# Performance work log

Hardware: AMD Instinct MI355X
Metric: run time of the kernel (lower is better)

## Reference

```python
import jax, jax.numpy as jnp
import numpy as np

# single species, e3tb basis 1s+1p+1d
FLIST = [1, 3, 5]           # flistnorbs (spin_factor = 1 pre-doubling)
NORB = 9                    # full_basis_norb
SPIN = 2                    # spin_deg -> block doubled
A, E, K = 192, 3072, 4
P = 58                      # sum_{i<=j} iorb*jorb = 1+3+5+9+15+25


def setup_inputs() -> dict:
    key = jax.random.key(0)
    ks = jax.random.split(key, 6)
    return dict(
        orbpair_hopping=jax.random.normal(ks[0], (E, P), jnp.float32),
        orbpair_onsite=jax.random.normal(ks[1], (A, P), jnp.float32),
        R_matrix=jax.random.normal(ks[2], (A, SPIN * NORB, SPIN * NORB), jnp.float32) * 0.1,
        kpoints=jax.random.uniform(ks[3], (K, 3), jnp.float32),
        edge_cell_shift=jax.random.normal(ks[4], (E, 3), jnp.float32),
        edge_index=jax.random.randint(ks[5], (2, E), 0, A, jnp.int64),
    )


def _assemble(feats):
    """Scatter flat orbpair features into upper-triangular [*, NORB, NORB] blocks."""
    n = feats.shape[0]
    H = jnp.zeros((n, NORB, NORB), feats.dtype)
    offs = np.concatenate([[0], np.cumsum(FLIST)])
    p = 0
    for i in range(len(FLIST)):
        for j in range(i, len(FLIST)):
            io, jo = FLIST[i], FLIST[j]
            f = 0.5 if i == j else 1.0  # diagonal orbpairs get 0.5 (hermitianized later)
            H = H.at[:, offs[i]:offs[i] + io, offs[j]:offs[j] + jo].set(
                f * feats[:, p:p + io * jo].reshape(n, io, jo))
            p += io * jo
    return H


def _spin_double(H):
    # H[:, :, 0, :, 0] = H[:, :, 1, :, 1] = H  (kron with eye(2), interleaved layout)
    n = H.shape[0]
    return jnp.einsum('aij,st->aisjt', H, jnp.eye(2, dtype=H.dtype)).reshape(n, SPIN * NORB, SPIN * NORB)


def reference(orbpair_hopping, orbpair_onsite, R_matrix, kpoints, edge_cell_shift, edge_index):
    s = SPIN * NORB
    src, dst = edge_index[0], edge_index[1]

    onsite = _spin_double(_assemble(orbpair_onsite))      # [A, s, s]
    hop = _spin_double(_assemble(orbpair_hopping))        # [E, s, s]

    # rotate: R @ H @ R^T (gathered per-edge for hoppings)
    onsite = jnp.einsum('aip,apq,ajq->aij', R_matrix, onsite, R_matrix)
    hop = jnp.einsum('eip,epq,ejq->eij', R_matrix[src], hop, R_matrix[dst])

    # Bloch phases exp(-2*pi*i k.S) per (k, edge)
    phase = jnp.exp(-2j * jnp.pi * (kpoints @ edge_cell_shift.T)).astype(jnp.complex64)  # [K, E]

    contrib = hop[None].astype(jnp.complex64) * phase[:, :, None, None]  # [K, E, s, s]
    pair = src * A + dst
    blk = jax.vmap(lambda c: jax.ops.segment_sum(c, pair, num_segments=A * A))(contrib)
    blk = blk.reshape(K, A, A, s, s)

    idx = jnp.arange(A)
    blk = blk.at[:, idx, idx].add(onsite[None].astype(jnp.complex64))  # onsite on diag, all k

    Hk = blk.transpose(0, 1, 3, 2, 4).reshape(K, A * s, A * s)
    return Hk + jnp.conj(jnp.swapaxes(Hk, 1, 2))
```

## Files before the change

kernel.cpp:

```cpp
#include <hip/hip_runtime.h>

#define PFEAT 58
#define S18   18
#define ENT   324
#define MAXE  128
#define MAXA  256

__device__ __constant__ unsigned char c_row[PFEAT] = {
    0,0,0,0,0,0,0,0,0,
    1,1,1,2,2,2,3,3,3,
    1,1,1,1,1,2,2,2,2,2,3,3,3,3,3,
    4,4,4,4,4,5,5,5,5,5,6,6,6,6,6,7,7,7,7,7,8,8,8,8,8};
__device__ __constant__ unsigned char c_col[PFEAT] = {
    0,1,2,3,4,5,6,7,8,
    1,2,3,1,2,3,1,2,3,
    4,5,6,7,8,4,5,6,7,8,4,5,6,7,8,
    4,5,6,7,8,4,5,6,7,8,4,5,6,7,8,4,5,6,7,8,4,5,6,7,8};
__device__ __constant__ float c_fac[PFEAT] = {
    0.5f,1,1,1,1,1,1,1,1,
    0.5f,0.5f,0.5f,0.5f,0.5f,0.5f,0.5f,0.5f,0.5f,
    1,1,1,1,1,1,1,1,1,1,1,1,1,1,1,
    0.5f,0.5f,0.5f,0.5f,0.5f,0.5f,0.5f,0.5f,0.5f,0.5f,0.5f,0.5f,0.5f,
    0.5f,0.5f,0.5f,0.5f,0.5f,0.5f,0.5f,0.5f,0.5f,0.5f,0.5f,0.5f};

__device__ __forceinline__ bool detect_i64(const int* __restrict__ ei) {
    const uint2* p = (const uint2*)ei;
    unsigned acc = 0u;
#pragma unroll 8
    for (int m = 0; m < 64; ++m) acc |= p[m].y;
    return acc == 0u;
}

__device__ __forceinline__ int load_idx(const int* __restrict__ ei, int pos,
                                        bool is64, int A) {
    int v = is64 ? ei[2 * pos] : ei[pos];
    v = v < 0 ? 0 : (v >= A ? A - 1 : v);
    return v;
}

__device__ __forceinline__ void assemble_rotate(
    const float* __restrict__ feat, const float* __restrict__ Rs,
    const float* __restrict__ Rd, float* sH9, float* sRs, float* sRd,
    float* sT, float* sM, int t, int nthreads)
{
    for (int idx = t; idx < ENT; idx += nthreads) { sRs[idx] = Rs[idx]; sRd[idx] = Rd[idx]; }
    if (t < 81) sH9[t] = 0.f;
    __syncthreads();
    if (t < PFEAT) sH9[c_row[t] * 9 + c_col[t]] = c_fac[t] * feat[t];
    __syncthreads();

    for (int idx = t; idx < ENT; idx += nthreads) {
        const int pp = idx / S18, q = idx - pp * S18;
        const int i = pp >> 1, u = pp & 1;
        float acc = 0.f;
#pragma unroll
        for (int j = 0; j < 9; ++j)
            acc += sH9[i * 9 + j] * sRd[q * S18 + 2 * j + u];
        sT[idx] = acc;
    }
    __syncthreads();

    for (int idx = t; idx < ENT; idx += nthreads) {
        const int p = idx / S18, q = idx - p * S18;
        float acc = 0.f;
#pragma unroll
        for (int pp = 0; pp < S18; ++pp)
            acc += sRs[p * S18 + pp] * sT[pp * S18 + q];
        sM[idx] = acc;
    }
}


__global__ __launch_bounds__(128) void prep_kernel(
    const float* __restrict__ hop_feat, const float* __restrict__ ons_feat,
    const float* __restrict__ R, const int* __restrict__ ei,
    const float* __restrict__ kpts, const float* __restrict__ shift,
    float* __restrict__ hop_rot, float* __restrict__ hop_rotT,
    float* __restrict__ ons_rot, float* __restrict__ pcos,
    float* __restrict__ psin, int* __restrict__ offsets,
    int2* __restrict__ entries, int E, int A, int K, int hasT)
{
    __shared__ float sH9[81];
    __shared__ float sRs[ENT];
    __shared__ float sRd[ENT];
    __shared__ float sT[ENT];
    __shared__ float sM[ENT];
    __shared__ int   scnt[MAXA];
    __shared__ int   scur[MAXA];
    __shared__ int   sflag;

    const int item = blockIdx.x;
    const int t = threadIdx.x;
    if (t == 0) sflag = detect_i64(ei) ? 1 : 0;
    __syncthreads();
    const bool s64 = sflag != 0;

    if (item == E + A) {
        for (int a = t; a < A; a += 128) scnt[a] = 0;
        __syncthreads();
        for (int e = t; e < E; e += 128) {
            const int a = load_idx(ei, e, s64, A);
            const int b = load_idx(ei, E + e, s64, A);
            atomicAdd(&scnt[a], 1);
            atomicAdd(&scnt[b], 1);
        }
        __syncthreads();
        if (t == 0) {
            int acc = 0;
            for (int a = 0; a < A; ++a) { scur[a] = acc; offsets[a] = acc; acc += scnt[a]; }
            offsets[A] = acc;
        }
        __syncthreads();
        for (int e = t; e < E; e += 128) {
            const int a = load_idx(ei, e, s64, A);
            const int b = load_idx(ei, E + e, s64, A);
            const int p = atomicAdd(&scur[a], 1);
            entries[p] = make_int2(e, b);
            const int q = atomicAdd(&scur[b], 1);
            entries[q] = make_int2(e | (1 << 30), a);
        }
        return;
    }

    const float* feat; const float* Rs; const float* Rd; float* outp;
    if (item < E) {
        const int a_s = load_idx(ei, item, s64, A);
        const int a_d = load_idx(ei, E + item, s64, A);
        feat = hop_feat + (size_t)item * PFEAT;
        Rs = R + (size_t)a_s * ENT;
        Rd = R + (size_t)a_d * ENT;
        outp = hop_rot + (size_t)item * ENT;
        for (int k = t; k < K; k += 128) {
            const float dot = kpts[k * 3 + 0] * shift[3 * item + 0]
                            + kpts[k * 3 + 1] * shift[3 * item + 1]
                            + kpts[k * 3 + 2] * shift[3 * item + 2];
            float sv, cv;
            sincosf(-6.28318530717958647692f * dot, &sv, &cv);
            pcos[item * K + k] = cv;
            psin[item * K + k] = sv;
        }
    } else {
        const int a = item - E;
        feat = ons_feat + (size_t)a * PFEAT;
        Rs = R + (size_t)a * ENT;
        Rd = Rs;
        outp = ons_rot + (size_t)a * ENT;
    }

    assemble_rotate(feat, Rs, Rd, sH9, sRs, sRd, sT, sM, t, 128);
    __syncthreads();

    for (int idx = t; idx < ENT; idx += 128) outp[idx] = sM[idx];
    if (item < E && hasT) {
        float* outpT = hop_rotT + (size_t)item * ENT;
        for (int idx = t; idx < ENT; idx += 128) {
            const int p = idx / S18, q = idx - p * S18;
            outpT[idx] = sM[q * S18 + p];
        }
    }
}

template <int KK>
__global__ __launch_bounds__(256) void writer_colsK_kernel(
    const float* __restrict__ hop_rot,
    const float* __restrict__ hop_rotT,
    const float* __restrict__ ons_rot,
    const int*   __restrict__ offsets,
    const int2*  __restrict__ entries,
    const float* __restrict__ pcos,
    float* __restrict__ outf,
    int A, long long lim)
{
    __shared__ int   se[MAXE];
    __shared__ int   sb[MAXE];
    __shared__ float spc[MAXE][KK];
    __shared__ float sons[ENT];

    const int N = A * S18;
    const long long N2 = (long long)N * N;
    const int a = blockIdx.y;
    const int t = threadIdx.x;
    const int c = blockIdx.x * 256 + t;

    const int beg = offsets[a];
    const int cnt = offsets[a + 1] - beg;
    const int nst = cnt < MAXE ? cnt : MAXE;
    for (int n = t; n < nst; n += 256) {
        const int2 ent = entries[beg + n];
        se[n] = ent.x;
        sb[n] = ent.y;
        const int e0 = ent.x & 0x3FFFFFFF;
#pragma unroll
        for (int k = 0; k < KK; ++k) spc[n][k] = pcos[e0 * KK + k];
    }
    for (int idx = t; idx < ENT; idx += 256) sons[idx] = ons_rot[a * ENT + idx];
    __syncthreads();

    if (c >= N) return;
    const int b = c / S18, l = c - b * S18;

    float acc[KK][S18];
#pragma unroll
    for (int k = 0; k < KK; ++k)
#pragma unroll
        for (int i = 0; i < S18; ++i) acc[k][i] = 0.f;

    if (b == a) {
#pragma unroll
        for (int i = 0; i < S18; ++i) {
            const float v = sons[i * S18 + l] + sons[l * S18 + i];
#pragma unroll
            for (int k = 0; k < KK; ++k) acc[k][i] = v;
        }
    }

    for (int n = 0; n < nst; ++n) {
        if (sb[n] != b) continue;
        const int ex = se[n];
        const int e = ex & 0x3FFFFFFF;
        const float* base = ((ex >> 30) & 1)
                          ? (hop_rot  + (size_t)e * ENT + l * S18)
                          : (hop_rotT + (size_t)e * ENT + l * S18);
        float v[S18];
#pragma unroll
        for (int i = 0; i < S18; ++i) v[i] = base[i];
#pragma unroll
        for (int k = 0; k < KK; ++k) {
            const float pc = spc[n][k];
#pragma unroll
            for (int i = 0; i < S18; ++i) acc[k][i] += v[i] * pc;
        }
    }
    for (int n = MAXE; n < cnt; ++n) {
        const int2 ent = entries[beg + n];
        if (ent.y != b) continue;
        const int e = ent.x & 0x3FFFFFFF;
        const float* base = ((ent.x >> 30) & 1)
                          ? (hop_rot  + (size_t)e * ENT + l * S18)
                          : (hop_rotT + (size_t)e * ENT + l * S18);
        float v[S18];
#pragma unroll
        for (int i = 0; i < S18; ++i) v[i] = base[i];
#pragma unroll
        for (int k = 0; k < KK; ++k) {
            const float pc = pcos[e * KK + k];
#pragma unroll
            for (int i = 0; i < S18; ++i) acc[k][i] += v[i] * pc;
        }
    }

    const long long colbase = (long long)a * S18 * N + c;
#pragma unroll
    for (int k = 0; k < KK; ++k) {
        const long long kb = (long long)k * N2 + colbase;
#pragma unroll
        for (int i = 0; i < S18; ++i) {
            const long long off = kb + (long long)i * N;
            if (off < lim) outf[off] = acc[k][i];
        }
    }
}

__global__ __launch_bounds__(384) void writer_cols_kernel(
    const float* __restrict__ hop_rot, const float* __restrict__ hop_rotT,
    const float* __restrict__ ons_rot, const int* __restrict__ offsets,
    const int2* __restrict__ entries, const float* __restrict__ pcos,
    float* __restrict__ outf, int A, int K, long long lim)
{
    __shared__ int   se[MAXE];
    __shared__ int   sb[MAXE];
    __shared__ float spc[MAXE];
    __shared__ float sons[ENT];

    const int N = A * S18;
    const int a = blockIdx.z;
    const int k = blockIdx.y;
    const int t = threadIdx.x;
    const int c = blockIdx.x * 384 + t;

    const int beg = offsets[a];
    const int cnt = offsets[a + 1] - beg;
    const int nst = cnt < MAXE ? cnt : MAXE;
    for (int n = t; n < nst; n += 384) {
        const int2 ent = entries[beg + n];
        se[n] = ent.x;
        sb[n] = ent.y;
        spc[n] = pcos[(ent.x & 0x3FFFFFFF) * K + k];
    }
    for (int idx = t; idx < ENT; idx += 384) sons[idx] = ons_rot[a * ENT + idx];
    __syncthreads();

    if (c >= N) return;
    const int b = c / S18, l = c - b * S18;

    float acc[S18];
    if (b == a) {
#pragma unroll
        for (int i = 0; i < S18; ++i)
            acc[i] = sons[i * S18 + l] + sons[l * S18 + i];
    } else {
#pragma unroll
        for (int i = 0; i < S18; ++i) acc[i] = 0.f;
    }

    for (int n = 0; n < nst; ++n) {
        if (sb[n] != b) continue;
        const int ex = se[n];
        const int e = ex & 0x3FFFFFFF;
        const float pc = spc[n];
        const float* base = ((ex >> 30) & 1)
                          ? (hop_rot  + (size_t)e * ENT + l * S18)
                          : (hop_rotT + (size_t)e * ENT + l * S18);
#pragma unroll
        for (int i = 0; i < S18; ++i) acc[i] += base[i] * pc;
    }
    for (int n = MAXE; n < cnt; ++n) {
        const int2 ent = entries[beg + n];
        if (ent.y != b) continue;
        const int e = ent.x & 0x3FFFFFFF;
        const float pc = pcos[e * K + k];
        const float* base = ((ent.x >> 30) & 1)
                          ? (hop_rot  + (size_t)e * ENT + l * S18)
                          : (hop_rotT + (size_t)e * ENT + l * S18);
#pragma unroll
        for (int i = 0; i < S18; ++i) acc[i] += base[i] * pc;
    }

    const long long rowbase = ((long long)k * N + (long long)a * S18) * (long long)N + c;
#pragma unroll
    for (int i = 0; i < S18; ++i) {
        const long long off = rowbase + (long long)i * N;
        if (off < lim) outf[off] = acc[i];
    }
}

__global__ __launch_bounds__(256) void write_kernel(
    const float* __restrict__ hop_rot, const float* __restrict__ hop_rotT,
    const float* __restrict__ ons_rot, const int* __restrict__ offsets,
    const int2* __restrict__ entries, const float* __restrict__ pcos,
    const float* __restrict__ psin, float* __restrict__ outf,
    int A, int K, int cplx, int hasT, long long lim)
{
    extern __shared__ float rowbuf[];
    __shared__ int2  sent[MAXE];
    __shared__ float sphc[MAXE];
    __shared__ float sphs[MAXE];
    __shared__ float sons[ENT];

    const int N = A * S18;
    const int a    = blockIdx.x >> 1;
    const int half = blockIdx.x & 1;
    const int k = blockIdx.y;
    const int t = threadIdx.x;
    const int i0 = half * 9;
    const int stride = cplx ? 2 : 1;
    const int nbuf = stride * N;
    const int nbuf4 = nbuf >> 2;

    const int beg = offsets[a], end = offsets[a + 1];
    const int cnt = end - beg;
    const int nst = cnt < MAXE ? cnt : MAXE;
    for (int n = t; n < nst; n += 256) {
        const int2 ent = entries[beg + n];
        sent[n] = ent;
        const int e0 = ent.x & 0x3FFFFFFF;
        sphc[n] = pcos[e0 * K + k];
        if (cplx) sphs[n] = psin[e0 * K + k];
    }
    for (int idx = t; idx < ENT; idx += 256) sons[idx] = ons_rot[a * ENT + idx];
    __syncthreads();

    float4* rb4 = (float4*)rowbuf;
    const int total = cnt * S18;

    for (int ri = 0; ri < 9; ++ri) {
        const int i = i0 + ri;
        for (int idx = t; idx < nbuf4; idx += 256)
            rb4[idx] = make_float4(0.f, 0.f, 0.f, 0.f);
        __syncthreads();

        if (t < S18)
            atomicAdd(&rowbuf[stride * (a * S18 + t)],
                      sons[i * S18 + t] + sons[t * S18 + i]);

        for (int m = t; m < total; m += 256) {
            const int n = m / S18, l = m - n * S18;
            int2 ent; float pc, ps = 0.f;
            if (n < MAXE) {
                ent = sent[n]; pc = sphc[n]; if (cplx) ps = sphs[n];
            } else {
                ent = entries[beg + n];
                const int e0 = ent.x & 0x3FFFFFFF;
                pc = pcos[e0 * K + k]; if (cplx) ps = psin[e0 * K + k];
            }
            const int conjf = (ent.x >> 30) & 1;
            const int e = ent.x & 0x3FFFFFFF;
            const int b = ent.y;
            float v;
            if (!conjf)     v = hop_rot [(size_t)e * ENT + i * S18 + l];
            else if (hasT)  v = hop_rotT[(size_t)e * ENT + i * S18 + l];
            else            v = hop_rot [(size_t)e * ENT + l * S18 + i];
            atomicAdd(&rowbuf[stride * (b * S18 + l)], v * pc);
            if (cplx)
                atomicAdd(&rowbuf[stride * (b * S18 + l) + 1], conjf ? -v * ps : v * ps);
        }
        __syncthreads();

        const long long base = (long long)stride
                             * ((long long)k * N + (long long)a * S18 + i)
                             * (long long)N;
        float* dst = outf + base;
        if (base + nbuf <= lim && ((base & 3) == 0)) {
            float4* d4 = (float4*)dst;
            for (int idx = t; idx < nbuf4; idx += 256) d4[idx] = rb4[idx];
        } else {
            for (int idx = t; idx < nbuf; idx += 256)
                if (base + idx < lim) dst[idx] = rowbuf[idx];
        }
        __syncthreads();
    }
}


__global__ __launch_bounds__(256) void zero_kernel(float* __restrict__ p, long long n)
{
    const long long i4 = ((long long)blockIdx.x * 256 + threadIdx.x) * 4;
    if (i4 + 3 < n) {
        *(float4*)(p + i4) = make_float4(0.f, 0.f, 0.f, 0.f);
    } else if (i4 < n) {
        for (long long i = i4; i < n; ++i) p[i] = 0.f;
    }
}

__global__ __launch_bounds__(256) void edge_kernel(
    const float* __restrict__ hop_feat, const float* __restrict__ R,
    const float* __restrict__ kpts, const float* __restrict__ shift,
    const int* __restrict__ edge_index, float* __restrict__ outf,
    int E, int A, int K, int cplx, long long lim)
{
    __shared__ float sH9[81];
    __shared__ float sRs[ENT];
    __shared__ float sRd[ENT];
    __shared__ float sT[ENT];
    __shared__ float sM[ENT];
    __shared__ float sC[8];
    __shared__ float sS[8];

    const int e = blockIdx.x;
    const int t = threadIdx.x;
    const int N = A * S18;
    const long long N2 = (long long)N * N;

    const bool is64 = detect_i64(edge_index);
    const int a = load_idx(edge_index, e, is64, A);
    const int b = load_idx(edge_index, E + e, is64, A);

    if (t < K && t < 8) {
        const float sx = shift[e * 3 + 0], sy = shift[e * 3 + 1], sz = shift[e * 3 + 2];
        const float dot = kpts[t * 3 + 0] * sx + kpts[t * 3 + 1] * sy + kpts[t * 3 + 2] * sz;
        float sv, cv;
        sincosf(-6.28318530717958647692f * dot, &sv, &cv);
        sC[t] = cv; sS[t] = sv;
    }

    assemble_rotate(hop_feat + (size_t)e * PFEAT,
                    R + (size_t)a * ENT, R + (size_t)b * ENT,
                    sH9, sRs, sRd, sT, sM, t, 256);
    __syncthreads();

    const int total = K * ENT;
    for (int idx = t; idx < total; idx += 256) {
        const int k = idx / ENT, r = idx - k * ENT;
        const int i = r / S18, j = r - i * S18;
        const float v = sM[r];
        const float re = v * sC[k];
        const float im = v * sS[k];
        const long long I = (long long)a * S18 + i;
        const long long J = (long long)b * S18 + j;
        const long long p1 = k * N2 + I * N + J;
        const long long p2 = k * N2 + J * N + I;
        if (cplx) {
            if (2 * p1 + 1 < lim) { atomicAdd(&outf[2 * p1], re); atomicAdd(&outf[2 * p1 + 1], im); }
            if (2 * p2 + 1 < lim) { atomicAdd(&outf[2 * p2], re); atomicAdd(&outf[2 * p2 + 1], -im); }
        } else {
            if (p1 < lim) atomicAdd(&outf[p1], re);
            if (p2 < lim) atomicAdd(&outf[p2], re);
        }
    }
}

__global__ __launch_bounds__(128) void onsite_kernel(
    const float* __restrict__ ons_feat, const float* __restrict__ R,
    float* __restrict__ outf, int A, int K, int cplx, long long lim)
{
    __shared__ float sH9[81];
    __shared__ float sRs[ENT];
    __shared__ float sRd[ENT];
    __shared__ float sT[ENT];
    __shared__ float sM[ENT];

    const int a = blockIdx.x;
    const int t = threadIdx.x;
    const int N = A * S18;
    const long long N2 = (long long)N * N;

    assemble_rotate(ons_feat + (size_t)a * PFEAT,
                    R + (size_t)a * ENT, R + (size_t)a * ENT,
                    sH9, sRs, sRd, sT, sM, t, 128);
    __syncthreads();

    for (int idx = t; idx < ENT; idx += 128) {
        const int i = idx / S18, j = idx - (idx / S18) * S18;
        const float v = sM[i * S18 + j] + sM[j * S18 + i];
        const long long I = (long long)a * S18 + i;
        const long long J = (long long)a * S18 + j;
        for (int k = 0; k < K; ++k) {
            const long long p1 = k * N2 + I * N + J;
            const long long off = cplx ? 2 * p1 : p1;
            if (off < lim) outf[off] += v;
        }
    }
}

extern "C" void kernel_launch(void* const* d_in, const int* in_sizes, int n_in,
                              void* d_out, int out_size, void* d_ws, size_t ws_size,
                              hipStream_t stream) {
    const float* hop_feat   = (const float*)d_in[0];
    const float* ons_feat   = (const float*)d_in[1];
    const float* R          = (const float*)d_in[2];
    const float* kpts       = (const float*)d_in[3];
    const float* shift      = (const float*)d_in[4];
    const int*   edge_index = (const int*)d_in[5];

    const int E = in_sizes[0] / PFEAT;
    const int A = in_sizes[1] / PFEAT;
    const int K = in_sizes[3] / 3;

    const long long N  = (long long)A * S18;
    const long long n_real = (long long)K * N * N;
    const long long lim = (long long)out_size;
    const int cplx = (lim >= 2 * n_real) ? 1 : 0;

    float* outf = (float*)d_out;

    char* ws = (char*)d_ws;
    const size_t off_hop = 0;
    const size_t off_ons = off_hop + (size_t)E * ENT * 4;
    const size_t off_ent = off_ons + (size_t)A * ENT * 4;
    const size_t off_off = off_ent + (size_t)2 * E * 8;
    const size_t off_pc  = off_off + (size_t)(A + 2) * 4;
    const size_t off_ps  = off_pc  + (size_t)E * K * 4;
    const size_t base_need = off_ps + (size_t)E * K * 4;
    const size_t off_hT  = base_need;
    const size_t full_need = off_hT + (size_t)E * ENT * 4;

    if (ws_size >= base_need && A <= MAXA) {
        const int hasT = (ws_size >= full_need) ? 1 : 0;
        float* hop_rot  = (float*)(ws + off_hop);
        float* ons_rot  = (float*)(ws + off_ons);
        int2*  entries  = (int2*)(ws + off_ent);
        int*   offsets  = (int*)(ws + off_off);
        float* pcos     = (float*)(ws + off_pc);
        float* psin     = (float*)(ws + off_ps);
        float* hop_rotT = (float*)(ws + off_hT);

        prep_kernel<<<E + A + 1, 128, 0, stream>>>(
            hop_feat, ons_feat, R, edge_index, kpts, shift,
            hop_rot, hop_rotT, ons_rot, pcos, psin, offsets, entries,
            E, A, K, hasT);

        if (cplx == 0 && hasT && K >= 1 && K <= 4) {
            const int nchunks = (int)((N + 255) / 256);
            dim3 grid((unsigned)nchunks, (unsigned)A);
            switch (K) {
            case 1: writer_colsK_kernel<1><<<grid, 256, 0, stream>>>(
                        hop_rot, hop_rotT, ons_rot, offsets, entries, pcos, outf, A, lim); break;
            case 2: writer_colsK_kernel<2><<<grid, 256, 0, stream>>>(
                        hop_rot, hop_rotT, ons_rot, offsets, entries, pcos, outf, A, lim); break;
            case 3: writer_colsK_kernel<3><<<grid, 256, 0, stream>>>(
                        hop_rot, hop_rotT, ons_rot, offsets, entries, pcos, outf, A, lim); break;
            default: writer_colsK_kernel<4><<<grid, 256, 0, stream>>>(
                        hop_rot, hop_rotT, ons_rot, offsets, entries, pcos, outf, A, lim); break;
            }
        } else if (cplx == 0 && hasT) {
            const int nchunks = (int)((N + 383) / 384);
            dim3 grid((unsigned)nchunks, (unsigned)K, (unsigned)A);
            writer_cols_kernel<<<grid, 384, 0, stream>>>(
                hop_rot, hop_rotT, ons_rot, offsets, entries, pcos,
                outf, A, K, lim);
        } else {
            const size_t shmem = (size_t)(cplx ? 2 : 1) * N * sizeof(float);
            dim3 grid((unsigned)(A * 2), (unsigned)K);
            write_kernel<<<grid, 256, shmem, stream>>>(hop_rot, hop_rotT, ons_rot,
                                                       offsets, entries, pcos, psin,
                                                       outf, A, K, cplx, hasT, lim);
        }
    } else {
        const long long n4 = (lim + 3) / 4;
        const int zgrid = (int)((n4 + 255) / 256);
        zero_kernel<<<zgrid, 256, 0, stream>>>(outf, lim);
        edge_kernel<<<E, 256, 0, stream>>>(hop_feat, R, kpts, shift, edge_index,
                                           outf, E, A, K, cplx, lim);
        onsite_kernel<<<A, 128, 0, stream>>>(ons_feat, R, outf, A, K, cplx, lim);
    }
}
```

Measured before the change: 223.3 us.

## Bucket per-row CSR entries by destination block to avoid scanning all entries

Adds a sort kernel that counting-sorts each atom row's edge entries by destination block and records per-block start offsets. A new writer kernel then has each column thread loop only over the entries for its own block and accumulate in registers, instead of scanning the whole row's list held in shared memory. This cuts the redundant per-thread filtering, at the cost of an extra kernel launch, more workspace, and large register arrays (KK*18 accumulators) that may lower occupancy.

```diff
diff --git a/kernel.cpp b/kernel.cpp
--- a/kernel.cpp
+++ b/kernel.cpp
@@ -5,6 +5,7 @@
 #define ENT   324
 #define MAXE  128
 #define MAXA  256
+#define SCAP  512
 
 __device__ __constant__ unsigned char c_row[PFEAT] = {
     0,0,0,0,0,0,0,0,0,
@@ -160,16 +161,139 @@
     }
 }
 
+__global__ __launch_bounds__(64) void sortcsr_kernel(
+    const int*  __restrict__ offsets,
+    const int2* __restrict__ entries,
+    int2* __restrict__ entries_s,
+    int*  __restrict__ bstart,
+    int A)
+{
+    __shared__ int2 sent[SCAP];
+    __shared__ int  sbin[MAXA];
+    __shared__ int  scur[MAXA];
+
+    const int a = blockIdx.x;
+    const int t = threadIdx.x;
+    const int beg = offsets[a];
+    const int cnt = offsets[a + 1] - beg;
+    int* row = bstart + a * (A + 1);
+
+    if (cnt > SCAP) {
+        for (int n = t; n < cnt; n += 64) entries_s[beg + n] = entries[beg + n];
+        if (t == 0) row[0] = -1;
+        return;
+    }
+
+    for (int b = t; b < A; b += 64) sbin[b] = 0;
+    for (int n = t; n < cnt; n += 64) sent[n] = entries[beg + n];
+    __syncthreads();
+    for (int n = t; n < cnt; n += 64) atomicAdd(&sbin[sent[n].y], 1);
+    __syncthreads();
+    if (t == 0) {
+        int acc = 0;
+        for (int b = 0; b < A; ++b) {
+            const int c0 = sbin[b];
+            sbin[b] = acc; scur[b] = acc;
+            acc += c0;
+        }
+    }
+    __syncthreads();
+    for (int b = t; b < A; b += 64) row[b] = beg + sbin[b];
+    if (t == 0) row[A] = beg + cnt;
+    for (int n = t; n < cnt; n += 64) {
+        const int2 ent = sent[n];
+        const int pos = atomicAdd(&scur[ent.y], 1);
+        entries_s[beg + pos] = ent;
+    }
+}
+
 template <int KK>
-__global__ __launch_bounds__(256) void writer_colsK_kernel(
+__global__ __launch_bounds__(256) void writer_sorted_kernel(
     const float* __restrict__ hop_rot,
     const float* __restrict__ hop_rotT,
     const float* __restrict__ ons_rot,
     const int*   __restrict__ offsets,
-    const int2*  __restrict__ entries,
+    const int2*  __restrict__ entries_s,
+    const int*   __restrict__ bstart,
     const float* __restrict__ pcos,
     float* __restrict__ outf,
     int A, long long lim)
+{
+    const int N = A * S18;
+    const long long N2 = (long long)N * N;
+    const int a = blockIdx.y;
+    const int c = blockIdx.x * 256 + threadIdx.x;
+    if (c >= N) return;
+    const int b = c / S18, l = c - b * S18;
+
+    float acc[KK][S18];
+#pragma unroll
+    for (int k = 0; k < KK; ++k)
+#pragma unroll
+        for (int i = 0; i < S18; ++i) acc[k][i] = 0.f;
+
+    if (b == a) {
+        const float* O = ons_rot + (size_t)a * ENT;
+#pragma unroll
+        for (int i = 0; i < S18; ++i) {
+            const float v = O[i * S18 + l] + O[l * S18 + i];
+#pragma unroll
+            for (int k = 0; k < KK; ++k) acc[k][i] = v;
+        }
+    }
+
+    const int* row = bstart + a * (A + 1);
+    int nbeg, nend; bool filt;
+    if (row[0] == -1) { nbeg = offsets[a]; nend = offsets[a + 1]; filt = true; }
+    else             { nbeg = row[b];     nend = row[b + 1];      filt = false; }
+
+    for (int n = nbeg; n < nend; ++n) {
+        const int2 ent = entries_s[n];
+        if (filt && ent.y != b) continue;
+        const int ex = ent.x;
+        const int e = ex & 0x3FFFFFFF;
+        const float* base = ((ex >> 30) & 1)
+                          ? (hop_rot  + (size_t)e * ENT + l * S18)
+                          : (hop_rotT + (size_t)e * ENT + l * S18);
+        float v[S18];
+#pragma unroll
+        for (int i = 0; i < S18; ++i) v[i] = base[i];
+#pragma unroll
+        for (int k = 0; k < KK; ++k) {
+            const float pc = pcos[e * KK + k];
+#pragma unroll
+            for (int i = 0; i < S18; ++i) acc[k][i] += v[i] * pc;
+        }
+    }
+
+    const long long colbase = (long long)a * S18 * N + c;
+    const long long maxoff = colbase + (long long)(KK - 1) * N2 + (long long)(S18 - 1) * N;
+    if (maxoff < lim) {
+#pragma unroll
+        for (int k = 0; k < KK; ++k) {
+            const long long kb = (long long)k * N2 + colbase;
+#pragma unroll
+            for (int i = 0; i < S18; ++i) outf[kb + (long long)i * N] = acc[k][i];
+        }
+    } else {
+#pragma unroll
+        for (int k = 0; k < KK; ++k) {
+            const long long kb = (long long)k * N2 + colbase;
+#pragma unroll
+            for (int i = 0; i < S18; ++i) {
+                const long long off = kb + (long long)i * N;
+                if (off < lim) outf[off] = acc[k][i];
+            }
+        }
+    }
+}
+
+template <int KK>
+__global__ __launch_bounds__(256) void writer_colsK_kernel(
+    const float* __restrict__ hop_rot, const float* __restrict__ hop_rotT,
+    const float* __restrict__ ons_rot, const int* __restrict__ offsets,
+    const int2* __restrict__ entries, const float* __restrict__ pcos,
+    float* __restrict__ outf, int A, long long lim)
 {
     __shared__ int   se[MAXE];
     __shared__ int   sb[MAXE];
@@ -553,23 +677,48 @@
     const size_t base_need = off_ps + (size_t)E * K * 4;
     const size_t off_hT  = base_need;
     const size_t full_need = off_hT + (size_t)E * ENT * 4;
+    const size_t off_es  = full_need;
+    const size_t off_bs  = off_es + (size_t)2 * E * 8;
+    const size_t sorted_need = off_bs + (size_t)A * (A + 1) * 4;
 
     if (ws_size >= base_need && A <= MAXA) {
         const int hasT = (ws_size >= full_need) ? 1 : 0;
-        float* hop_rot  = (float*)(ws + off_hop);
-        float* ons_rot  = (float*)(ws + off_ons);
-        int2*  entries  = (int2*)(ws + off_ent);
-        int*   offsets  = (int*)(ws + off_off);
-        float* pcos     = (float*)(ws + off_pc);
-        float* psin     = (float*)(ws + off_ps);
-        float* hop_rotT = (float*)(ws + off_hT);
+        const int hasS = (ws_size >= sorted_need) ? 1 : 0;
+        float* hop_rot   = (float*)(ws + off_hop);
+        float* ons_rot   = (float*)(ws + off_ons);
+        int2*  entries   = (int2*)(ws + off_ent);
+        int*   offsets   = (int*)(ws + off_off);
+        float* pcos      = (float*)(ws + off_pc);
+        float* psin      = (float*)(ws + off_ps);
+        float* hop_rotT  = (float*)(ws + off_hT);
+        int2*  entries_s = (int2*)(ws + off_es);
+        int*   bstart    = (int*)(ws + off_bs);
 
         prep_kernel<<<E + A + 1, 128, 0, stream>>>(
             hop_feat, ons_feat, R, edge_index, kpts, shift,
             hop_rot, hop_rotT, ons_rot, pcos, psin, offsets, entries,
             E, A, K, hasT);
 
-        if (cplx == 0 && hasT && K >= 1 && K <= 4) {
+        if (cplx == 0 && hasT && hasS && K >= 1 && K <= 4) {
+            sortcsr_kernel<<<A, 64, 0, stream>>>(offsets, entries, entries_s,
+                                                 bstart, A);
+            const int nchunks = (int)((N + 255) / 256);
+            dim3 grid((unsigned)nchunks, (unsigned)A);
+            switch (K) {
+            case 1: writer_sorted_kernel<1><<<grid, 256, 0, stream>>>(
+                        hop_rot, hop_rotT, ons_rot, offsets, entries_s, bstart,
+                        pcos, outf, A, lim); break;
+            case 2: writer_sorted_kernel<2><<<grid, 256, 0, stream>>>(
+                        hop_rot, hop_rotT, ons_rot, offsets, entries_s, bstart,
+                        pcos, outf, A, lim); break;
+            case 3: writer_sorted_kernel<3><<<grid, 256, 0, stream>>>(
+                        hop_rot, hop_rotT, ons_rot, offsets, entries_s, bstart,
+                        pcos, outf, A, lim); break;
+            default: writer_sorted_kernel<4><<<grid, 256, 0, stream>>>(
+                        hop_rot, hop_rotT, ons_rot, offsets, entries_s, bstart,
+                        pcos, outf, A, lim); break;
+            }
+        } else if (cplx == 0 && hasT && K >= 1 && K <= 4) {
             const int nchunks = (int)((N + 255) / 256);
             dim3 grid((unsigned)nchunks, (unsigned)A);
             switch (K) {
```

After: 226.8 us. About the same (+1.6%).
